# Kernel tuning notes

Measured on AMD Instinct MI355X. Metric: run time of the kernel, lower is better.

## Reference

```python
import jax, jax.numpy as jnp
import numpy as np

N = 50000      # nodes
E = 400000     # edges (before self-loops)
G = 256        # graphs in batch
H = 2          # attention heads
C = 100        # out channels per head
F_IN = 336
SLOPE = 0.2    # PyG GATConv default negative_slope


def setup_inputs() -> dict:
    key = jax.random.key(0)
    ks = jax.random.split(key, 32)
    inp = {}
    inp['x'] = jax.random.normal(ks[0], (N, F_IN), dtype=jnp.float32)
    inp['edge_index'] = jax.random.randint(ks[1], (2, E), 0, N, dtype=jnp.int32)
    inp['batch'] = jnp.sort(jax.random.randint(ks[2], (N,), 0, G, dtype=jnp.int32))
    dims = [F_IN, 200, 200, 200, 200]
    k = 3
    for i in range(5):
        d = dims[i]
        inp[f'W{i+1}'] = jax.random.normal(ks[k], (d, H * C), dtype=jnp.float32) / float(np.sqrt(d)); k += 1
        inp[f'asrc{i+1}'] = jax.random.normal(ks[k], (H, C), dtype=jnp.float32) * 0.1; k += 1
        inp[f'adst{i+1}'] = jax.random.normal(ks[k], (H, C), dtype=jnp.float32) * 0.1; k += 1
        inp[f'bc{i+1}'] = jnp.zeros((H * C,), jnp.float32)
    for i, (a, b) in enumerate([(200, 100), (100, 100), (100, 29)]):
        inp[f'lw{i+1}'] = jax.random.normal(ks[k], (a, b), dtype=jnp.float32) / float(np.sqrt(a)); k += 1
        inp[f'lb{i+1}'] = jnp.zeros((b,), jnp.float32)
    return inp


def _gat(x, src, dst, W, a_s, a_d, b):
    # PyG GATConv (concat=True): per-head linear, additive attention,
    # softmax over incoming edges per destination node, weighted sum.
    h = (x @ W).reshape(-1, H, C)                      # [N,H,C]
    es = jnp.einsum('nhc,hc->nh', h, a_s)              # [N,H] src scores
    ed = jnp.einsum('nhc,hc->nh', h, a_d)              # [N,H] dst scores
    e = jax.nn.leaky_relu(es[src] + ed[dst], SLOPE)    # [E+N,H]
    m = jax.ops.segment_max(e, dst, num_segments=N)    # per-dest max (stable softmax)
    p = jnp.exp(e - m[dst])
    s = jax.ops.segment_sum(p, dst, num_segments=N)
    alpha = p / (s[dst] + 1e-16)                       # [E+N,H]
    msg = alpha[:, :, None] * h[src]                   # [E+N,H,C]
    out = jax.ops.segment_sum(msg, dst, num_segments=N)
    return out.reshape(-1, H * C) + b


def reference(x, edge_index, batch,
              W1, asrc1, adst1, bc1, W2, asrc2, adst2, bc2,
              W3, asrc3, adst3, bc3, W4, asrc4, adst4, bc4,
              W5, asrc5, adst5, bc5,
              lw1, lb1, lw2, lb2, lw3, lb3):
    loop = jnp.arange(N, dtype=edge_index.dtype)       # self-loops (PyG default)
    src = jnp.concatenate([edge_index[0], loop])
    dst = jnp.concatenate([edge_index[1], loop])
    for W, a_s, a_d, b in [(W1, asrc1, adst1, bc1), (W2, asrc2, adst2, bc2),
                           (W3, asrc3, adst3, bc3), (W4, asrc4, adst4, bc4),
                           (W5, asrc5, adst5, bc5)]:
        x = jax.nn.relu(_gat(x, src, dst, W, a_s, a_d, b))
    # global mean pool over nodes of each graph
    sums = jax.ops.segment_sum(x, batch, num_segments=G)
    cnt = jax.ops.segment_sum(jnp.ones((N, 1), x.dtype), batch, num_segments=G)
    x = sums / jnp.maximum(cnt, 1.0)
    x = jax.nn.relu(x @ lw1 + lb1)
    x = jax.nn.relu(x @ lw2 + lb2)
    return x @ lw3 + lb3
```

## Files before the change

kernel.cpp:

```cpp
#include <hip/hip_runtime.h>
#include <hip/hip_bf16.h>
#include <math.h>

#define F_IN   336
#define HC     200
#define Cch    100
#define SLOPE  0.2f
#define SCAN_BS 256

#define NPAD   224
#define KP0    352
#define KP1    224

using short8   = __attribute__((ext_vector_type(8))) short;
using float4v  = __attribute__((ext_vector_type(4))) float;
using ushort4v = __attribute__((ext_vector_type(4))) unsigned short;
using float2v  = __attribute__((ext_vector_type(2))) float;

__device__ inline unsigned short rne_bf16(float v) {
    unsigned int u = __float_as_uint(v);
    return (unsigned short)((u + 0x7fffu + ((u >> 16) & 1u)) >> 16);
}
__device__ inline void split_bf(float v, unsigned short& hi, unsigned short& lo) {
    hi = rne_bf16(v);
    float hv = __uint_as_float(((unsigned int)hi) << 16);
    lo = rne_bf16(v - hv);
}

__device__ inline unsigned int enc_f32(float f) {
    unsigned int u = __float_as_uint(f);
    return (u & 0x80000000u) ? ~u : (u | 0x80000000u);
}
__device__ inline float dec_f32(unsigned int e) {
    return __uint_as_float((e & 0x80000000u) ? (e ^ 0x80000000u) : ~e);
}

__global__ void init_deg(int* deg, unsigned int* gmax, int n) {
    int i = blockIdx.x * 256 + threadIdx.x;
    if (i < n) deg[i] = 1;
    if (i < 10) gmax[i] = 0x007FFFFFu;
}

__global__ void count_deg(const int* __restrict__ dst, int* deg, int e) {
    int i = blockIdx.x * 256 + threadIdx.x;
    if (i < e) atomicAdd(&deg[dst[i]], 1);
}

__global__ void scan_block(const int* __restrict__ deg, int* incl, int* bsums, int n) {
    __shared__ int sm[SCAN_BS];
    int i = blockIdx.x * SCAN_BS + threadIdx.x;
    int v = (i < n) ? deg[i] : 0;
    sm[threadIdx.x] = v;
    __syncthreads();
    for (int off = 1; off < SCAN_BS; off <<= 1) {
        int t = (threadIdx.x >= off) ? sm[threadIdx.x - off] : 0;
        __syncthreads();
        sm[threadIdx.x] += t;
        __syncthreads();
    }
    if (i < n) incl[i] = sm[threadIdx.x];
    if (threadIdx.x == SCAN_BS - 1) bsums[blockIdx.x] = sm[threadIdx.x];
}

__global__ void scan_sums(int* bsums, int nb) {
    __shared__ int sm[SCAN_BS];
    int v = (threadIdx.x < nb) ? bsums[threadIdx.x] : 0;
    sm[threadIdx.x] = v;
    __syncthreads();
    for (int off = 1; off < SCAN_BS; off <<= 1) {
        int t = (threadIdx.x >= off) ? sm[threadIdx.x - off] : 0;
        __syncthreads();
        sm[threadIdx.x] += t;
        __syncthreads();
    }
    if (threadIdx.x < nb) bsums[threadIdx.x] = sm[threadIdx.x] - v;
}

__global__ void scan_final(const int* __restrict__ incl, const int* __restrict__ deg,
                           const int* __restrict__ bsums, int* row_ptr, int* cursor, int n) {
    int i = blockIdx.x * SCAN_BS + threadIdx.x;
    if (i < n) {
        int inc = incl[i] + bsums[i / SCAN_BS];
        int ex  = inc - deg[i];
        row_ptr[i] = ex;
        cursor[i]  = ex;
        if (i == n - 1) row_ptr[n] = inc;
    }
}

__global__ void fill_csr(const int* __restrict__ src, const int* __restrict__ dst,
                         int* cursor, int* col_src, int e, int n) {
    int i = blockIdx.x * 256 + threadIdx.x;
    int te = e + n;
    if (i >= te) return;
    int s, d;
    if (i < e) { s = src[i]; d = dst[i]; }
    else       { s = i - e;  d = i - e; }
    int pos = atomicAdd(&cursor[d], 1);
    col_src[pos] = s;
}

__global__ void conv_x(const float* __restrict__ x, unsigned short* __restrict__ Ah,
                       unsigned short* __restrict__ Al, int n_nodes) {
    const int GPR = KP0 / 4;
    int i = blockIdx.x * 256 + threadIdx.x;
    int tot = n_nodes * GPR;
    if (i >= tot) return;
    int row = i / GPR, g4 = i - row * GPR;
    int col = g4 * 4;
    float4v v = {0.f, 0.f, 0.f, 0.f};
    if (col < F_IN) v = *(const float4v*)(x + (size_t)row * F_IN + col);
    ushort4v hv, lv;
    split_bf(v.x, ((unsigned short*)&hv)[0], ((unsigned short*)&lv)[0]);
    split_bf(v.y, ((unsigned short*)&hv)[1], ((unsigned short*)&lv)[1]);
    split_bf(v.z, ((unsigned short*)&hv)[2], ((unsigned short*)&lv)[2]);
    split_bf(v.w, ((unsigned short*)&hv)[3], ((unsigned short*)&lv)[3]);
    size_t b = (size_t)row * KP0 + col;
    *(ushort4v*)(Ah + b) = hv;
    *(ushort4v*)(Al + b) = lv;
}

__global__ void conv_w_all(const float* __restrict__ W0, const float* __restrict__ W1,
                           const float* __restrict__ W2, const float* __restrict__ W3,
                           const float* __restrict__ W4,
                           unsigned short* __restrict__ Bh, unsigned short* __restrict__ Bl) {
    const int SZ0 = NPAD * KP0, SZ = NPAD * KP1;
    const int TOT = SZ0 + 4 * SZ;
    int i = blockIdx.x * 256 + threadIdx.x;
    if (i >= TOT) return;
    const float* W; int Kp, K, idx;
    if (i < SZ0) { W = W0; Kp = KP0; K = F_IN; idx = i; }
    else {
        int j = i - SZ0; int l = j / SZ; idx = j - l * SZ;
        W = (l == 0) ? W1 : (l == 1) ? W2 : (l == 2) ? W3 : W4;
        Kp = KP1; K = HC;
    }
    int n = idx / Kp, k = idx - n * Kp;
    float v = (n < HC && k < K) ? W[(size_t)k * HC + n] : 0.f;
    unsigned short hi, lo;
    split_bf(v, hi, lo);
    Bh[i] = hi; Bl[i] = lo;
}

#define LDK 40
__global__ __launch_bounds__(256, 2) void gemm_split(
    const unsigned short* __restrict__ Ah, const unsigned short* __restrict__ Al,
    const unsigned short* __restrict__ Bh, const unsigned short* __restrict__ Bl,
    const float* __restrict__ asrc, const float* __restrict__ adst,
    float* __restrict__ h, float* __restrict__ es, float* __restrict__ ed,
    unsigned int* __restrict__ gmax,
    int M, int Kp)
{
    __shared__ unsigned short As[2][64][LDK];
    __shared__ unsigned short Bs[2][NPAD][LDK];
    __shared__ float sc[64][4];
    int tid  = threadIdx.x;
    int wave = tid >> 6, lane = tid & 63;
    int quad = lane >> 4, l16 = lane & 15;
    int wm = (wave >> 1) * 32;
    int wn = (wave & 1) * 112;
    int r0 = blockIdx.x * 64;

    ((float*)sc)[tid] = 0.f;

    float4v acc[2][7];
#pragma unroll
    for (int mt = 0; mt < 2; mt++)
#pragma unroll
        for (int nt = 0; nt < 7; nt++)
            acc[mt][nt] = (float4v){0.f, 0.f, 0.f, 0.f};

    for (int k0 = 0; k0 < Kp; k0 += 32) {
#pragma unroll
        for (int i = 0; i < 2; i++) {
            int c = tid + 256 * i;
            int s = c >> 8;
            int cc = c & 255;
            int row = cc >> 2, kc = (cc & 3) * 8;
            const unsigned short* g = s ? Al : Ah;
            uint4 v = make_uint4(0u, 0u, 0u, 0u);
            int gr = r0 + row;
            if (gr < M) v = *(const uint4*)(g + (size_t)gr * Kp + k0 + kc);
            *(uint4*)&As[s][row][kc] = v;
        }
#pragma unroll
        for (int i = 0; i < 7; i++) {
            int c = tid + 256 * i;
            int s = (c >= 896) ? 1 : 0;
            int cc = c - s * 896;
            int row = cc >> 2, kc = (cc & 3) * 8;
            const unsigned short* g = s ? Bl : Bh;
            *(uint4*)&Bs[s][row][kc] = *(const uint4*)(g + (size_t)row * Kp + k0 + kc);
        }
        __syncthreads();

        short8 a_h[2], a_l[2];
#pragma unroll
        for (int mt = 0; mt < 2; mt++) {
            a_h[mt] = *(const short8*)&As[0][wm + mt * 16 + l16][quad * 8];
            a_l[mt] = *(const short8*)&As[1][wm + mt * 16 + l16][quad * 8];
        }
#pragma unroll
        for (int nt = 0; nt < 7; nt++) {
            short8 b_h = *(const short8*)&Bs[0][wn + nt * 16 + l16][quad * 8];
            short8 b_l = *(const short8*)&Bs[1][wn + nt * 16 + l16][quad * 8];
#pragma unroll
            for (int mt = 0; mt < 2; mt++) {
                acc[mt][nt] = __builtin_amdgcn_mfma_f32_16x16x32_bf16(a_h[mt], b_h, acc[mt][nt], 0, 0, 0);
                acc[mt][nt] = __builtin_amdgcn_mfma_f32_16x16x32_bf16(a_h[mt], b_l, acc[mt][nt], 0, 0, 0);
                acc[mt][nt] = __builtin_amdgcn_mfma_f32_16x16x32_bf16(a_l[mt], b_h, acc[mt][nt], 0, 0, 0);
            }
        }
        __syncthreads();
    }

    float asc[7], adc[7];
    bool  vld[7];
    bool  hd1[7];
#pragma unroll
    for (int nt = 0; nt < 7; nt++) {
        int col = wn + nt * 16 + l16;
        vld[nt] = col < HC;
        hd1[nt] = col >= Cch;
        asc[nt] = vld[nt] ? asrc[col] : 0.f;
        adc[nt] = vld[nt] ? adst[col] : 0.f;
    }

#pragma unroll
    for (int mt = 0; mt < 2; mt++) {
        float p[4][4];
#pragma unroll
        for (int r = 0; r < 4; r++)
#pragma unroll
            for (int t = 0; t < 4; t++) p[r][t] = 0.f;
#pragma unroll
        for (int nt = 0; nt < 7; nt++) {
            int col = wn + nt * 16 + l16;
#pragma unroll
            for (int r = 0; r < 4; r++) {
                float v = acc[mt][nt][r];
                int grow = r0 + wm + mt * 16 + quad * 4 + r;
                if (vld[nt] && grow < M) h[(size_t)grow * HC + col] = v;
                float va = v * asc[nt], vd = v * adc[nt];
                p[r][0] += hd1[nt] ? 0.f : va;
                p[r][1] += hd1[nt] ? va  : 0.f;
                p[r][2] += hd1[nt] ? 0.f : vd;
                p[r][3] += hd1[nt] ? vd  : 0.f;
            }
        }
#pragma unroll
        for (int off = 1; off < 16; off <<= 1)
#pragma unroll
            for (int r = 0; r < 4; r++)
#pragma unroll
                for (int t = 0; t < 4; t++)
                    p[r][t] += __shfl_xor(p[r][t], off);
        if (l16 == 0) {
            int lrow = wm + mt * 16 + quad * 4;
#pragma unroll
            for (int r = 0; r < 4; r++)
#pragma unroll
                for (int t = 0; t < 4; t++)
                    atomicAdd(&sc[lrow + r][t], p[r][t]);
        }
    }
    __syncthreads();
    if (tid < 64) {
        int grow = r0 + tid;
        float e0v = sc[tid][0], e1v = sc[tid][1];
        if (grow < M) {
            es[grow * 2 + 0] = e0v;
            es[grow * 2 + 1] = e1v;
            ed[grow * 2 + 0] = sc[tid][2];
            ed[grow * 2 + 1] = sc[tid][3];
        }
#pragma unroll
        for (int off = 1; off < 64; off <<= 1) {
            e0v = fmaxf(e0v, __shfl_xor(e0v, off));
            e1v = fmaxf(e1v, __shfl_xor(e1v, off));
        }
        if (tid == 0) {
            atomicMax(&gmax[0], enc_f32(e0v));
            atomicMax(&gmax[1], enc_f32(e1v));
        }
    }
}

template<bool WF, bool WB>
__global__ __launch_bounds__(256) void gat_gather(
    const float* __restrict__ h, const float* __restrict__ es, const float* __restrict__ ed,
    const unsigned int* __restrict__ gmax,
    const int* __restrict__ row_ptr, const int* __restrict__ col_src,
    const float* __restrict__ bias, float* __restrict__ outF,
    unsigned short* __restrict__ oh, unsigned short* __restrict__ ol, int n_nodes)
{
    int wave = threadIdx.x >> 6, lane = threadIdx.x & 63;
    int n = blockIdx.x * 4 + wave;
    if (n >= n_nodes) return;
    int e0 = row_ptr[n], e1 = row_ptr[n + 1];
    bool act  = lane < 50;
    int  hsel = (lane >= 25) ? 1 : 0;
    float ed0 = ed[n * 2], ed1 = ed[n * 2 + 1];
    float gm0 = dec_f32(gmax[0]), gm1 = dec_f32(gmax[1]);
    float t0 = gm0 + ed0, t1 = gm1 + ed1;
    float mb0 = t0 > 0.f ? t0 : SLOPE * t0;
    float mb1 = t1 > 0.f ? t1 : SLOPE * t1;

    float l0 = 0.f, l1 = 0.f;
    float4v a0 = {0.f, 0.f, 0.f, 0.f}, a1 = {0.f, 0.f, 0.f, 0.f};
    float4v a2 = {0.f, 0.f, 0.f, 0.f}, a3 = {0.f, 0.f, 0.f, 0.f};

    for (int cbase = e0; cbase < e1; cbase += 64) {
        int cnt = e1 - cbase; if (cnt > 64) cnt = 64;
        int   sidx = 0;
        float px = 0.f, py = 0.f;
        if (lane < cnt) {
            sidx = col_src[cbase + lane];
            float2v q = *(const float2v*)&es[sidx * 2];
            float s0 = q.x + ed0, s1 = q.y + ed1;
            s0 = s0 > 0.f ? s0 : SLOPE * s0;
            s1 = s1 > 0.f ? s1 : SLOPE * s1;
            px = __expf(s0 - mb0);
            py = __expf(s1 - mb1);
            l0 += px; l1 += py;
        }
        int j = 0;
        for (; j + 4 <= cnt; j += 4) {
            int s0 = __shfl(sidx, j + 0), s1 = __shfl(sidx, j + 1);
            int s2 = __shfl(sidx, j + 2), s3 = __shfl(sidx, j + 3);
            float x0 = __shfl(px, j + 0), y0 = __shfl(py, j + 0);
            float x1 = __shfl(px, j + 1), y1 = __shfl(py, j + 1);
            float x2 = __shfl(px, j + 2), y2 = __shfl(py, j + 2);
            float x3 = __shfl(px, j + 3), y3 = __shfl(py, j + 3);
            float p0 = hsel ? y0 : x0;
            float p1 = hsel ? y1 : x1;
            float p2 = hsel ? y2 : x2;
            float p3 = hsel ? y3 : x3;
            if (act) {
                float4v v0 = *(const float4v*)(h + (size_t)s0 * HC + lane * 4);
                float4v v1 = *(const float4v*)(h + (size_t)s1 * HC + lane * 4);
                float4v v2 = *(const float4v*)(h + (size_t)s2 * HC + lane * 4);
                float4v v3 = *(const float4v*)(h + (size_t)s3 * HC + lane * 4);
                a0.x += p0 * v0.x; a0.y += p0 * v0.y; a0.z += p0 * v0.z; a0.w += p0 * v0.w;
                a1.x += p1 * v1.x; a1.y += p1 * v1.y; a1.z += p1 * v1.z; a1.w += p1 * v1.w;
                a2.x += p2 * v2.x; a2.y += p2 * v2.y; a2.z += p2 * v2.z; a2.w += p2 * v2.w;
                a3.x += p3 * v3.x; a3.y += p3 * v3.y; a3.z += p3 * v3.z; a3.w += p3 * v3.w;
            }
        }
        for (; j < cnt; j++) {
            int s0 = __shfl(sidx, j);
            float x0 = __shfl(px, j), y0 = __shfl(py, j);
            float p0 = hsel ? y0 : x0;
            if (act) {
                float4v v0 = *(const float4v*)(h + (size_t)s0 * HC + lane * 4);
                a0.x += p0 * v0.x; a0.y += p0 * v0.y; a0.z += p0 * v0.z; a0.w += p0 * v0.w;
            }
        }
    }
#pragma unroll
    for (int off = 1; off < 64; off <<= 1) {
        l0 += __shfl_xor(l0, off);
        l1 += __shfl_xor(l1, off);
    }

    float4v acc;
    acc.x = (a0.x + a1.x) + (a2.x + a3.x);
    acc.y = (a0.y + a1.y) + (a2.y + a3.y);
    acc.z = (a0.z + a1.z) + (a2.z + a3.z);
    acc.w = (a0.w + a1.w) + (a2.w + a3.w);

    float li = 1.f / ((hsel ? l1 : l0) + 1e-33f);
    if (act) {
        float4v bb = *(const float4v*)(bias + lane * 4);
        float4v r;
        r.x = fmaxf(acc.x * li + bb.x, 0.f);
        r.y = fmaxf(acc.y * li + bb.y, 0.f);
        r.z = fmaxf(acc.z * li + bb.z, 0.f);
        r.w = fmaxf(acc.w * li + bb.w, 0.f);
        if (WF) {
            __builtin_nontemporal_store(r, (float4v*)(outF + (size_t)n * HC + lane * 4));
        }
        if (WB) {
            ushort4v hv, lv;
            split_bf(r.x, ((unsigned short*)&hv)[0], ((unsigned short*)&lv)[0]);
            split_bf(r.y, ((unsigned short*)&hv)[1], ((unsigned short*)&lv)[1]);
            split_bf(r.z, ((unsigned short*)&hv)[2], ((unsigned short*)&lv)[2]);
            split_bf(r.w, ((unsigned short*)&hv)[3], ((unsigned short*)&lv)[3]);
            size_t b = (size_t)n * NPAD + lane * 4;
            __builtin_nontemporal_store(hv, (ushort4v*)(oh + b));
            __builtin_nontemporal_store(lv, (ushort4v*)(ol + b));
        }
    } else if (WB && lane < 56) {
        ushort4v z = {0, 0, 0, 0};
        size_t b = (size_t)n * NPAD + lane * 4;
        __builtin_nontemporal_store(z, (ushort4v*)(oh + b));
        __builtin_nontemporal_store(z, (ushort4v*)(ol + b));
    }
}

__global__ void bounds_zero(const int* __restrict__ batch, int* gstart,
                            float* pool, int n, int g) {
    int i = blockIdx.x * 256 + threadIdx.x;
    if (i < g * HC) pool[i] = 0.f;
    if (i >= n) return;
    int b = batch[i];
    int bp = (i == 0) ? -1 : batch[i - 1];
    for (int q = bp + 1; q <= b; q++) gstart[q] = i;
    if (i == n - 1) for (int q = b + 1; q <= g; q++) gstart[q] = n;
}

__global__ __launch_bounds__(256) void pool_part(
    const float* __restrict__ x, const int* __restrict__ batch,
    float* __restrict__ pool, int n_nodes)
{
    int wave = threadIdx.x >> 6, lane = threadIdx.x & 63;
    int base = (blockIdx.x * 4 + wave) * 16;
    if (base >= n_nodes) return;
    bool act = lane < 50;
    int end = base + 16; if (end > n_nodes) end = n_nodes;
    float4v acc = {0.f, 0.f, 0.f, 0.f};
    int curg = batch[base];
    for (int n = base; n < end; n++) {
        int g = batch[n];
        if (g != curg) {
            if (act) {
                float* pp = pool + (size_t)curg * HC + lane * 4;
                atomicAdd(pp + 0, acc.x); atomicAdd(pp + 1, acc.y);
                atomicAdd(pp + 2, acc.z); atomicAdd(pp + 3, acc.w);
            }
            acc = (float4v){0.f, 0.f, 0.f, 0.f};
            curg = g;
        }
        if (act) {
            float4v v = *(const float4v*)(x + (size_t)n * HC + lane * 4);
            acc.x += v.x; acc.y += v.y; acc.z += v.z; acc.w += v.w;
        }
    }
    if (act) {
        float* pp = pool + (size_t)curg * HC + lane * 4;
        atomicAdd(pp + 0, acc.x); atomicAdd(pp + 1, acc.y);
        atomicAdd(pp + 2, acc.z); atomicAdd(pp + 3, acc.w);
    }
}

__global__ __launch_bounds__(128) void mlp_head(
    const float* __restrict__ pool, const int* __restrict__ gstart,
    const float* __restrict__ lw1, const float* __restrict__ lb1,
    const float* __restrict__ lw2, const float* __restrict__ lb2,
    const float* __restrict__ lw3, const float* __restrict__ lb3,
    float* __restrict__ out)
{
    __shared__ float xa[200];
    __shared__ float xb[100];
    __shared__ float xc[100];
    int g = blockIdx.x, t = threadIdx.x;
    float inv = 1.f / fmaxf((float)(gstart[g + 1] - gstart[g]), 1.f);
    for (int k = t; k < 200; k += 128) xa[k] = pool[g * 200 + k] * inv;
    __syncthreads();
    if (t < 100) {
        float s = lb1[t];
        for (int k = 0; k < 200; k++) s = fmaf(xa[k], lw1[k * 100 + t], s);
        xb[t] = fmaxf(s, 0.f);
    }
    __syncthreads();
    if (t < 100) {
        float s = lb2[t];
        for (int k = 0; k < 100; k++) s = fmaf(xb[k], lw2[k * 100 + t], s);
        xc[t] = fmaxf(s, 0.f);
    }
    __syncthreads();
    if (t < 29) {
        float s = lb3[t];
        for (int k = 0; k < 100; k++) s = fmaf(xc[k], lw3[k * 29 + t], s);
        out[g * 29 + t] = s;
    }
}

extern "C" void kernel_launch(void* const* d_in, const int* in_sizes, int n_in,
                              void* d_out, int out_size, void* d_ws, size_t ws_size,
                              hipStream_t stream) {
    const float* x     = (const float*)d_in[0];
    const int*   ei    = (const int*)d_in[1];
    const int*   batch = (const int*)d_in[2];
    const float *W[5], *asrc[5], *adst[5], *bc[5];
    for (int i = 0; i < 5; i++) {
        W[i]    = (const float*)d_in[3 + i * 4];
        asrc[i] = (const float*)d_in[4 + i * 4];
        adst[i] = (const float*)d_in[5 + i * 4];
        bc[i]   = (const float*)d_in[6 + i * 4];
    }
    const float* lw1 = (const float*)d_in[23];
    const float* lb1 = (const float*)d_in[24];
    const float* lw2 = (const float*)d_in[25];
    const float* lb2 = (const float*)d_in[26];
    const float* lw3 = (const float*)d_in[27];
    const float* lb3 = (const float*)d_in[28];
    float* out = (float*)d_out;

    const int N  = in_sizes[0] / F_IN;
    const int E  = in_sizes[1] / 2;
    const int G  = out_size / 29;
    const int TE = E + N;
    const int* esrc = ei;
    const int* edst = ei + E;

    const int WSZ0 = NPAD * KP0;
    const int WSZ  = NPAD * KP1;
    const int WTOT = WSZ0 + 4 * WSZ;

    char* p = (char*)d_ws;
    auto carve = [&](size_t bytes) { void* r = (void*)p; p += ((bytes + 255) / 256) * 256; return r; };
    float*          hbuf = (float*)carve((size_t)N * HC * 4);
    unsigned short* Ah   = (unsigned short*)carve((size_t)N * KP0 * 2);
    unsigned short* Al   = (unsigned short*)carve((size_t)N * KP0 * 2);
    float*          outF = (float*)Ah;
    unsigned short* Wth  = (unsigned short*)carve((size_t)WTOT * 2);
    unsigned short* Wtl  = (unsigned short*)carve((size_t)WTOT * 2);
    float* es_     = (float*)carve((size_t)N * 2 * 4);
    float* ed_     = (float*)carve((size_t)N * 2 * 4);
    unsigned int* gmax5 = (unsigned int*)carve(10 * 4);
    int*   deg     = (int*)carve((size_t)N * 4);
    int*   incl    = (int*)carve((size_t)N * 4);
    int*   bsums   = (int*)carve(SCAN_BS * 4);
    int*   row_ptr = (int*)carve((size_t)(N + 1) * 4);
    int*   cursor  = (int*)carve((size_t)N * 4);
    int*   col_src = (int*)carve((size_t)TE * 4);
    int*   gstart  = (int*)carve((size_t)(G + 1) * 4);
    float* pool    = (float*)carve((size_t)G * HC * 4);

    const int nBlkN   = (N + 255) / 256;
    const int nBlkE   = (E + 255) / 256;
    const int nBlkTE  = (TE + 255) / 256;
    const int nScanB  = (N + SCAN_BS - 1) / SCAN_BS;
    const int nWaveB  = (N + 3) / 4;
    const int nGemmB  = (N + 63) / 64;
    const int nPoolB  = (N + 63) / 64;
    const int nBZ     = (((N > G * HC) ? N : G * HC) + 255) / 256;

    init_deg<<<nBlkN, 256, 0, stream>>>(deg, gmax5, N);
    count_deg<<<nBlkE, 256, 0, stream>>>(edst, deg, E);
    scan_block<<<nScanB, SCAN_BS, 0, stream>>>(deg, incl, bsums, N);
    scan_sums<<<1, SCAN_BS, 0, stream>>>(bsums, nScanB);
    scan_final<<<nScanB, SCAN_BS, 0, stream>>>(incl, deg, bsums, row_ptr, cursor, N);
    fill_csr<<<nBlkTE, 256, 0, stream>>>(esrc, edst, cursor, col_src, E, N);

    conv_x<<<(N * (KP0 / 4) + 255) / 256, 256, 0, stream>>>(x, Ah, Al, N);
    conv_w_all<<<(WTOT + 255) / 256, 256, 0, stream>>>(W[0], W[1], W[2], W[3], W[4], Wth, Wtl);

    for (int L = 0; L < 5; L++) {
        int Kp   = (L == 0) ? KP0 : KP1;
        int woff = (L == 0) ? 0 : WSZ0 + (L - 1) * WSZ;
        gemm_split<<<nGemmB, 256, 0, stream>>>(Ah, Al, Wth + woff, Wtl + woff,
                                               asrc[L], adst[L], hbuf, es_, ed_,
                                               gmax5 + 2 * L, N, Kp);
        if (L < 4)
            gat_gather<false, true><<<nWaveB, 256, 0, stream>>>(hbuf, es_, ed_, gmax5 + 2 * L,
                                                                row_ptr, col_src,
                                                                bc[L], nullptr, Ah, Al, N);
        else
            gat_gather<true, false><<<nWaveB, 256, 0, stream>>>(hbuf, es_, ed_, gmax5 + 2 * L,
                                                                row_ptr, col_src,
                                                                bc[L], outF, nullptr, nullptr, N);
    }

    bounds_zero<<<nBZ, 256, 0, stream>>>(batch, gstart, pool, N, G);
    pool_part<<<nPoolB, 256, 0, stream>>>(outF, batch, pool, N);
    mlp_head<<<G, 128, 0, stream>>>(pool, gstart, lw1, lb1, lw2, lb2, lw3, lb3, out);
}
```

Baseline: 844.3 us.

## Prefetch next GEMM K-tile into registers while computing current tile

The linear-projection GEMM kernel now loads the next 32-wide K slice of A and B from global memory into registers right after storing the current slice to shared memory, so those loads overlap the MFMA work. Global-to-shared thread mapping is also changed so consecutive threads cover consecutive rows, which alters the shared-memory store pattern. Address arithmetic is hoisted out of the K loop. The cost is more live registers (nine uint4s plus precomputed offsets), which may lower occupancy.

```diff
diff --git a/kernel.cpp b/kernel.cpp
--- a/kernel.cpp
+++ b/kernel.cpp
@@ -163,6 +163,28 @@
 
     ((float*)sc)[tid] = 0.f;
 
+    int a_s[2], a_row[2], a_kc[2]; bool a_v[2]; size_t a_go[2];
+#pragma unroll
+    for (int i = 0; i < 2; i++) {
+        int c = tid + 256 * i;
+        int s = c >> 8, cc = c & 255;
+        int row = cc & 63, kc = (cc >> 6) * 8;
+        a_s[i] = s; a_row[i] = row; a_kc[i] = kc;
+        int gr = r0 + row;
+        a_v[i]  = gr < M;
+        a_go[i] = (size_t)(a_v[i] ? gr : 0) * Kp + kc;
+    }
+    int b_s[7], b_row[7], b_kc[7]; size_t b_go[7];
+#pragma unroll
+    for (int i = 0; i < 7; i++) {
+        int c = tid + 256 * i;
+        int s = (c >= 896) ? 1 : 0;
+        int cc = c - s * 896;
+        int row = cc % 224, kc = (cc / 224) * 8;
+        b_s[i] = s; b_row[i] = row; b_kc[i] = kc;
+        b_go[i] = (size_t)row * Kp + kc;
+    }
+
     float4v acc[2][7];
 #pragma unroll
     for (int mt = 0; mt < 2; mt++)
@@ -170,29 +192,45 @@
         for (int nt = 0; nt < 7; nt++)
             acc[mt][nt] = (float4v){0.f, 0.f, 0.f, 0.f};
 
+    uint4 ra[2], rb[7];
+#pragma unroll
+    for (int i = 0; i < 2; i++) {
+        const unsigned short* g = a_s[i] ? Al : Ah;
+        uint4 v = make_uint4(0u, 0u, 0u, 0u);
+        if (a_v[i]) v = *(const uint4*)(g + a_go[i]);
+        ra[i] = v;
+    }
+#pragma unroll
+    for (int i = 0; i < 7; i++) {
+        const unsigned short* g = b_s[i] ? Bl : Bh;
+        rb[i] = *(const uint4*)(g + b_go[i]);
+    }
+
     for (int k0 = 0; k0 < Kp; k0 += 32) {
-#pragma unroll
-        for (int i = 0; i < 2; i++) {
-            int c = tid + 256 * i;
-            int s = c >> 8;
-            int cc = c & 255;
-            int row = cc >> 2, kc = (cc & 3) * 8;
-            const unsigned short* g = s ? Al : Ah;
-            uint4 v = make_uint4(0u, 0u, 0u, 0u);
-            int gr = r0 + row;
-            if (gr < M) v = *(const uint4*)(g + (size_t)gr * Kp + k0 + kc);
-            *(uint4*)&As[s][row][kc] = v;
-        }
-#pragma unroll
-        for (int i = 0; i < 7; i++) {
-            int c = tid + 256 * i;
-            int s = (c >= 896) ? 1 : 0;
-            int cc = c - s * 896;
-            int row = cc >> 2, kc = (cc & 3) * 8;
-            const unsigned short* g = s ? Bl : Bh;
-            *(uint4*)&Bs[s][row][kc] = *(const uint4*)(g + (size_t)row * Kp + k0 + kc);
-        }
         __syncthreads();
+#pragma unroll
+        for (int i = 0; i < 2; i++)
+            *(uint4*)&As[a_s[i]][a_row[i]][a_kc[i]] = ra[i];
+#pragma unroll
+        for (int i = 0; i < 7; i++)
+            *(uint4*)&Bs[b_s[i]][b_row[i]][b_kc[i]] = rb[i];
+        __syncthreads();
+
+        int kn = k0 + 32;
+        if (kn < Kp) {
+#pragma unroll
+            for (int i = 0; i < 2; i++) {
+                const unsigned short* g = a_s[i] ? Al : Ah;
+                uint4 v = make_uint4(0u, 0u, 0u, 0u);
+                if (a_v[i]) v = *(const uint4*)(g + a_go[i] + kn);
+                ra[i] = v;
+            }
+#pragma unroll
+            for (int i = 0; i < 7; i++) {
+                const unsigned short* g = b_s[i] ? Bl : Bh;
+                rb[i] = *(const uint4*)(g + b_go[i] + kn);
+            }
+        }
 
         short8 a_h[2], a_l[2];
 #pragma unroll
@@ -211,7 +249,6 @@
                 acc[mt][nt] = __builtin_amdgcn_mfma_f32_16x16x32_bf16(a_l[mt], b_h, acc[mt][nt], 0, 0, 0);
             }
         }
-        __syncthreads();
     }
 
     float asc[7], adc[7];
```

After: 1.075 ms. 27.4% more time.

## Double-buffer GEMM tiles via direct global-to-LDS loads with XOR swizzle

Applied to the files above, without the earlier changes.

Replaces the register-staged global loads into padded shared arrays with __builtin_amdgcn_global_load_lds that writes straight into two LDS buffers. The next K-slice is fetched while the current one feeds the MFMAs. An XOR swizzle on the 16-byte column chunk replaces the padding to avoid bank conflicts. Out-of-range rows are clamped to M-1 instead of zeroed, so the per-block max now masks invalid rows with -inf. The intent is to hide global load latency and cut VGPR traffic. It depends on the intrinsic's wave-uniform LDS base semantics and on correct barrier placement between the two buffers.

```diff
diff --git a/kernel.cpp b/kernel.cpp
--- a/kernel.cpp
+++ b/kernel.cpp
@@ -16,6 +16,9 @@
 using float4v  = __attribute__((ext_vector_type(4))) float;
 using ushort4v = __attribute__((ext_vector_type(4))) unsigned short;
 using float2v  = __attribute__((ext_vector_type(2))) float;
+
+typedef __attribute__((address_space(1))) const void GASV;
+typedef __attribute__((address_space(3))) void LASV;
 
 __device__ inline unsigned short rne_bf16(float v) {
     unsigned int u = __float_as_uint(v);
@@ -142,7 +145,7 @@
     Bh[i] = hi; Bl[i] = lo;
 }
 
-#define LDK 40
+#define LBUF 18432
 __global__ __launch_bounds__(256, 2) void gemm_split(
     const unsigned short* __restrict__ Ah, const unsigned short* __restrict__ Al,
     const unsigned short* __restrict__ Bh, const unsigned short* __restrict__ Bl,
@@ -151,8 +154,7 @@
     unsigned int* __restrict__ gmax,
     int M, int Kp)
 {
-    __shared__ unsigned short As[2][64][LDK];
-    __shared__ unsigned short Bs[2][NPAD][LDK];
+    __shared__ unsigned short Ls[2][LBUF];
     __shared__ float sc[64][4];
     int tid  = threadIdx.x;
     int wave = tid >> 6, lane = tid & 63;
@@ -163,6 +165,28 @@
 
     ((float*)sc)[tid] = 0.f;
 
+    const unsigned short* gp[9];
+    unsigned lof[9];
+    {
+        int r16 = lane >> 2;
+        int cl  = (lane & 3) ^ ((lane >> 3) & 3);
+#pragma unroll
+        for (int j = 0; j < 9; j++) {
+            int c = wave * 9 + j;
+            if (c < 8) {
+                int s = c >> 2, rb = (c & 3) * 16;
+                int gr = r0 + rb + r16; if (gr >= M) gr = M - 1;
+                gp[j]  = (s ? Al : Ah) + (size_t)gr * Kp + cl * 8;
+                lof[j] = s * 2048 + rb * 32;
+            } else {
+                int cb = c - 8;
+                int s = (cb >= 14) ? 1 : 0, rb = (cb - s * 14) * 16;
+                gp[j]  = (s ? Bl : Bh) + (size_t)(rb + r16) * Kp + cl * 8;
+                lof[j] = 4096 + s * 7168 + rb * 32;
+            }
+        }
+    }
+
     float4v acc[2][7];
 #pragma unroll
     for (int mt = 0; mt < 2; mt++)
@@ -170,40 +194,36 @@
         for (int nt = 0; nt < 7; nt++)
             acc[mt][nt] = (float4v){0.f, 0.f, 0.f, 0.f};
 
+#pragma unroll
+    for (int j = 0; j < 9; j++)
+        __builtin_amdgcn_global_load_lds((GASV*)(gp[j]), (LASV*)(&Ls[0][0] + lof[j]), 16, 0, 0);
+    __syncthreads();
+
     for (int k0 = 0; k0 < Kp; k0 += 32) {
-#pragma unroll
-        for (int i = 0; i < 2; i++) {
-            int c = tid + 256 * i;
-            int s = c >> 8;
-            int cc = c & 255;
-            int row = cc >> 2, kc = (cc & 3) * 8;
-            const unsigned short* g = s ? Al : Ah;
-            uint4 v = make_uint4(0u, 0u, 0u, 0u);
-            int gr = r0 + row;
-            if (gr < M) v = *(const uint4*)(g + (size_t)gr * Kp + k0 + kc);
-            *(uint4*)&As[s][row][kc] = v;
-        }
-#pragma unroll
-        for (int i = 0; i < 7; i++) {
-            int c = tid + 256 * i;
-            int s = (c >= 896) ? 1 : 0;
-            int cc = c - s * 896;
-            int row = cc >> 2, kc = (cc & 3) * 8;
-            const unsigned short* g = s ? Bl : Bh;
-            *(uint4*)&Bs[s][row][kc] = *(const uint4*)(g + (size_t)row * Kp + k0 + kc);
-        }
-        __syncthreads();
-
+        int cur = (k0 >> 5) & 1;
+        int kn  = k0 + 32;
+        if (kn < Kp) {
+            unsigned short* lb = &Ls[cur ^ 1][0];
+#pragma unroll
+            for (int j = 0; j < 9; j++)
+                __builtin_amdgcn_global_load_lds((GASV*)(gp[j] + kn), (LASV*)(lb + lof[j]), 16, 0, 0);
+        }
+
+        const unsigned short* Lc = &Ls[cur][0];
         short8 a_h[2], a_l[2];
 #pragma unroll
         for (int mt = 0; mt < 2; mt++) {
-            a_h[mt] = *(const short8*)&As[0][wm + mt * 16 + l16][quad * 8];
-            a_l[mt] = *(const short8*)&As[1][wm + mt * 16 + l16][quad * 8];
+            int row = wm + mt * 16 + l16;
+            int cph = (quad ^ ((row >> 1) & 3)) * 8;
+            a_h[mt] = *(const short8*)(Lc + row * 32 + cph);
+            a_l[mt] = *(const short8*)(Lc + 2048 + row * 32 + cph);
         }
 #pragma unroll
         for (int nt = 0; nt < 7; nt++) {
-            short8 b_h = *(const short8*)&Bs[0][wn + nt * 16 + l16][quad * 8];
-            short8 b_l = *(const short8*)&Bs[1][wn + nt * 16 + l16][quad * 8];
+            int row = wn + nt * 16 + l16;
+            int cph = (quad ^ ((row >> 1) & 3)) * 8;
+            short8 b_h = *(const short8*)(Lc + 4096 + row * 32 + cph);
+            short8 b_l = *(const short8*)(Lc + 11264 + row * 32 + cph);
 #pragma unroll
             for (int mt = 0; mt < 2; mt++) {
                 acc[mt][nt] = __builtin_amdgcn_mfma_f32_16x16x32_bf16(a_h[mt], b_h, acc[mt][nt], 0, 0, 0);
@@ -267,8 +287,10 @@
     __syncthreads();
     if (tid < 64) {
         int grow = r0 + tid;
-        float e0v = sc[tid][0], e1v = sc[tid][1];
-        if (grow < M) {
+        bool v = grow < M;
+        float e0v = v ? sc[tid][0] : -INFINITY;
+        float e1v = v ? sc[tid][1] : -INFINITY;
+        if (v) {
             es[grow * 2 + 0] = e0v;
             es[grow * 2 + 1] = e1v;
             ed[grow * 2 + 0] = sc[tid][2];
```

Result: no change. 835.2 us (-1.1%).
